# Optimization experiments

Measured on AMD Instinct MI355X. Metric: run time of the kernel, lower is better.

## Reference

```python
import jax, jax.numpy as jnp
import numpy as np

N = 8192
E = 131072
IN_DIM = 3000
HID = 512      # gcn1 out = HID // 2 = 256
OUT = 64
EPS = 1e-12


def gcn_conv(x, W, b, src, dst, n):
    """PyG GCNConv: add self-loops, symmetric norm, gather-matmul-scatter."""
    xw = x @ W                                   # [n, out]
    loop = jnp.arange(n, dtype=src.dtype)
    s = jnp.concatenate([src, loop])             # source j
    d = jnp.concatenate([dst, loop])             # target i
    deg = jax.ops.segment_sum(jnp.ones(s.shape[0], dtype=xw.dtype), d, num_segments=n)
    dinv = deg ** -0.5                           # deg >= 1 due to self-loops
    norm = dinv[s] * dinv[d]                     # [E+n]
    out = jax.ops.segment_sum(norm[:, None] * xw[s], d, num_segments=n)
    return out + b


def avg_readout(emb, mask):
    vsum = mask @ emb                            # [N, h]
    row_sum = jnp.sum(mask, axis=1, keepdims=True)
    g = vsum / row_sum
    nrm = jnp.maximum(jnp.linalg.norm(g, axis=1, keepdims=True), EPS)
    return g / nrm                               # F.normalize(p=2, dim=1)


def bilinear(h, c, Wd, bd):
    # nn.Bilinear(n_h, n_h, 1): out[n,o] = sum_ij h[n,i] Wd[o,i,j] c[n,j] + bd[o]
    return jnp.einsum('ni,oij,nj->no', h, Wd, c) + bd


def setup_inputs() -> dict:
    key = jax.random.key(0)
    k1, k2, k3, k4, k5, k6, k7 = jax.random.split(key, 7)
    gene_data = jax.random.normal(k1, (N, IN_DIM), dtype=jnp.float32)
    # sparse binary neighborhood mask (~16 neighbors/row) + self so row sums > 0
    mask = (jax.random.uniform(k2, (N, N)) < (16.0 / N)).astype(jnp.float32)
    mask = jnp.maximum(mask, jnp.eye(N, dtype=jnp.float32))
    spatial_edge_index = jax.random.randint(k3, (2, E), 0, N, dtype=jnp.int64)
    perm = jax.random.permutation(k4, N).astype(jnp.int64)
    h1 = HID // 2
    W1 = jax.random.normal(k5, (IN_DIM, h1), dtype=jnp.float32) / np.sqrt(IN_DIM)
    b1 = jnp.zeros((h1,), dtype=jnp.float32)
    W2 = jax.random.normal(k6, (h1, OUT), dtype=jnp.float32) / np.sqrt(h1)
    b2 = jnp.zeros((OUT,), dtype=jnp.float32)
    Wd = jax.random.normal(k7, (1, OUT, OUT), dtype=jnp.float32) / np.sqrt(OUT)
    bd = jnp.zeros((1,), dtype=jnp.float32)
    return {"gene_data": gene_data, "mask": mask, "W1": W1, "b1": b1,
            "W2": W2, "b2": b2, "Wd": Wd, "bd": bd,
            "spatial_edge_index": spatial_edge_index, "perm": perm}


def reference(gene_data, mask, W1, b1, W2, b2, Wd, bd, spatial_edge_index, perm):
    src, dst = spatial_edge_index[0], spatial_edge_index[1]
    n = gene_data.shape[0]
    x1 = gene_data
    x1_c = gene_data[perm]                       # permuted (corrupted) graph
    # dropout inactive (eval mode, p=0.0)
    x1 = jax.nn.relu(gcn_conv(x1, W1, b1, src, dst, n))
    x1_c = jax.nn.relu(gcn_conv(x1_c, W1, b1, src, dst, n))
    x1 = jax.nn.relu(gcn_conv(x1, W2, b2, src, dst, n))
    x1_c = jax.nn.relu(gcn_conv(x1_c, W2, b2, src, dst, n))
    g1 = jax.nn.sigmoid(avg_readout(x1, mask))
    g1_c = jax.nn.sigmoid(avg_readout(x1_c, mask))
    ret1 = jnp.concatenate([bilinear(x1, g1, Wd, bd), bilinear(x1_c, g1, Wd, bd)], axis=1)
    ret1_c = jnp.concatenate([bilinear(x1_c, g1_c, Wd, bd), bilinear(x1, g1_c, Wd, bd)], axis=1)
    return (x1, ret1, ret1_c)
```

## Files before the change

kernel.cpp:

```cpp
#include <hip/hip_runtime.h>
#include <hip/hip_bf16.h>

#define NN 8192
#define NMASK 8191
#define IND 3000
#define H1 256
#define OUTD 64

typedef __bf16 bf16x8 __attribute__((ext_vector_type(8)));
typedef float floatx4 __attribute__((ext_vector_type(4)));

__device__ __forceinline__ unsigned short f2b(float f) {
    __hip_bfloat16 h = __float2bfloat16(f);
    unsigned short u;
    __builtin_memcpy(&u, &h, 2);
    return u;
}


__global__ void k_probe(float code, float* out) {
    if (threadIdx.x == 0 && blockIdx.x == 0) out[0] = code;
}


__global__ void k_detect64(const unsigned* __restrict__ raw, int pairs, int* __restrict__ flag) {
    __shared__ int cnt;
    if (threadIdx.x == 0) cnt = 0;
    __syncthreads();
    int z = 0;
    for (int k = threadIdx.x; k < pairs; k += blockDim.x)
        if (raw[2 * k + 1] == 0u) z++;
    atomicAdd(&cnt, z);
    __syncthreads();
    if (threadIdx.x == 0) *flag = (cnt > pairs / 2) ? 1 : 0;
}

__global__ void k_norm_idx(const unsigned* __restrict__ raw, const int* __restrict__ flag,
                           int* __restrict__ out, int count) {
    int i = blockIdx.x * blockDim.x + threadIdx.x;
    if (i < count) {
        unsigned v = (*flag) ? raw[2 * (size_t)i] : raw[i];
        out[i] = (int)(v & (unsigned)NMASK);
    }
}


__global__ void k_degree(const int* __restrict__ dst, int* __restrict__ deg, int E) {
    int e = blockIdx.x * blockDim.x + threadIdx.x;
    if (e < E) atomicAdd(&deg[dst[e]], 1);
}

__global__ __launch_bounds__(1024) void k_scan(const int* __restrict__ deg,
                                               int* __restrict__ row_ptr,
                                               int* __restrict__ cursor,
                                               float* __restrict__ dinv, int n) {
    __shared__ int sums[1024];
    int t = threadIdx.x;
    int per = n / 1024;
    int base = t * per;
    int s = 0;
    for (int u = 0; u < per; ++u) s += deg[base + u];
    sums[t] = s;
    __syncthreads();
    for (int off = 1; off < 1024; off <<= 1) {
        int v = (t >= off) ? sums[t - off] : 0;
        __syncthreads();
        sums[t] += v;
        __syncthreads();
    }
    int run = (t == 0) ? 0 : sums[t - 1];
    for (int u = 0; u < per; ++u) {
        int i = base + u;
        row_ptr[i] = run;
        cursor[i] = run;
        int d = deg[i];
        dinv[i] = rsqrtf((float)(1 + d));
        run += d;
    }
    if (t == 1023) row_ptr[n] = run;
}

__global__ void k_scatter(const int* __restrict__ src, const int* __restrict__ dst,
                          int* __restrict__ cursor, int* __restrict__ col, int E) {
    int e = blockIdx.x * blockDim.x + threadIdx.x;
    if (e < E) {
        int d = dst[e];
        int p = atomicAdd(&cursor[d], 1);
        if (p >= 0 && p < E) col[p] = src[e];
    }
}

__global__ void k_transpose_f2b(const float* __restrict__ in,
                                __hip_bfloat16* __restrict__ out, int R, int C) {
    int idx = blockIdx.x * blockDim.x + threadIdx.x;
    if (idx < R * C) {
        int r = idx / C, c = idx % C;
        out[(size_t)c * R + r] = __float2bfloat16(in[idx]);
    }
}


template <int AFP32>
__global__ __launch_bounds__(256) void k_gemm_bt(const void* __restrict__ Araw,
                                                 const __hip_bfloat16* __restrict__ Bt,
                                                 float* __restrict__ C,
                                                 int M, int N, int K) {
    __shared__ __align__(16) unsigned short As[64 * 40];
    __shared__ __align__(16) unsigned short Bs[64 * 40];
    int t = threadIdx.x;
    int m0 = blockIdx.x * 64;
    int n0 = blockIdx.y * 64;
    int lane = t & 63;
    int w = t >> 6;
    int srow = t >> 2;
    int schunk = (t & 3) * 8;
    size_t aoff = (size_t)(m0 + srow) * K + schunk;
    const unsigned short* Brow = (const unsigned short*)Bt + (size_t)(n0 + srow) * K + schunk;

    floatx4 acc0 = {0.f, 0.f, 0.f, 0.f}, acc1 = acc0, acc2 = acc0, acc3 = acc0;
    int msub = w * 16;
    int arow = msub + (lane & 15);
    int koff = (lane >> 4) * 8;
    int nlo = lane & 15;

    for (int k0 = 0; k0 < K; k0 += 32) {
        uint4 av = make_uint4(0u, 0u, 0u, 0u);
        uint4 bv = make_uint4(0u, 0u, 0u, 0u);
        if (k0 + schunk < K) {
            if (AFP32) {
                const float* ap = (const float*)Araw + aoff + k0;
                float4 f0 = *reinterpret_cast<const float4*>(ap);
                float4 f1 = *reinterpret_cast<const float4*>(ap + 4);
                unsigned short t8[8] = {f2b(f0.x), f2b(f0.y), f2b(f0.z), f2b(f0.w),
                                        f2b(f1.x), f2b(f1.y), f2b(f1.z), f2b(f1.w)};
                __builtin_memcpy(&av, t8, 16);
            } else {
                av = *reinterpret_cast<const uint4*>((const unsigned short*)Araw + aoff + k0);
            }
            bv = *reinterpret_cast<const uint4*>(Brow + k0);
        }
        __syncthreads();
        *reinterpret_cast<uint4*>(&As[srow * 40 + schunk]) = av;
        *reinterpret_cast<uint4*>(&Bs[srow * 40 + schunk]) = bv;
        __syncthreads();
        bf16x8 af = *reinterpret_cast<const bf16x8*>(&As[arow * 40 + koff]);
        bf16x8 bf0 = *reinterpret_cast<const bf16x8*>(&Bs[(0 + nlo) * 40 + koff]);
        bf16x8 bf1 = *reinterpret_cast<const bf16x8*>(&Bs[(16 + nlo) * 40 + koff]);
        bf16x8 bf2 = *reinterpret_cast<const bf16x8*>(&Bs[(32 + nlo) * 40 + koff]);
        bf16x8 bf3 = *reinterpret_cast<const bf16x8*>(&Bs[(48 + nlo) * 40 + koff]);
        acc0 = __builtin_amdgcn_mfma_f32_16x16x32_bf16(af, bf0, acc0, 0, 0, 0);
        acc1 = __builtin_amdgcn_mfma_f32_16x16x32_bf16(af, bf1, acc1, 0, 0, 0);
        acc2 = __builtin_amdgcn_mfma_f32_16x16x32_bf16(af, bf2, acc2, 0, 0, 0);
        acc3 = __builtin_amdgcn_mfma_f32_16x16x32_bf16(af, bf3, acc3, 0, 0, 0);
    }
    int crow = msub + (lane >> 4) * 4;
    int ccol = lane & 15;
    floatx4 accs[4] = {acc0, acc1, acc2, acc3};
#pragma unroll
    for (int j = 0; j < 4; ++j) {
#pragma unroll
        for (int r = 0; r < 4; ++r) {
            C[(size_t)(m0 + crow + r) * N + (n0 + j * 16 + ccol)] = accs[j][r];
        }
    }
}


__global__ __launch_bounds__(256) void k_agg1(const float* __restrict__ xw1,
                                              const int* __restrict__ row_ptr,
                                              const int* __restrict__ col,
                                              const float* __restrict__ dinv,
                                              const int* __restrict__ perm,
                                              const float* __restrict__ b1,
                                              __hip_bfloat16* __restrict__ h_all, int n) {
    __shared__ int colS[64];
    __shared__ int pcolS[64];
    __shared__ float wS[64];
    int i = blockIdx.x;
    int c = threadIdx.x;
    float di = dinv[i];
    int pi = perm[i];
    float sw = di * di;
    float acc = sw * xw1[(size_t)i * H1 + c];
    float accc = sw * xw1[(size_t)pi * H1 + c];
    int s = row_ptr[i], e = row_ptr[i + 1];
    for (int base = s; base < e; base += 64) {
        int cnt = min(64, e - base);
        __syncthreads();
        if (c < cnt) {
            int j = col[base + c];
            colS[c] = j;
            wS[c] = di * dinv[j];
            pcolS[c] = perm[j];
        }
        __syncthreads();
#pragma unroll 4
        for (int u = 0; u < cnt; ++u) {
            float wv = wS[u];
            acc += wv * xw1[(size_t)colS[u] * H1 + c];
            accc += wv * xw1[(size_t)pcolS[u] * H1 + c];
        }
    }
    float b = b1[c];
    h_all[(size_t)i * H1 + c] = __float2bfloat16(fmaxf(acc + b, 0.f));
    h_all[(size_t)(n + i) * H1 + c] = __float2bfloat16(fmaxf(accc + b, 0.f));
}


__global__ __launch_bounds__(256) void k_agg2(const float* __restrict__ hw_all,
                                              const int* __restrict__ row_ptr,
                                              const int* __restrict__ col,
                                              const float* __restrict__ dinv,
                                              const float* __restrict__ b2,
                                              float* __restrict__ x1_all,
                                              float* __restrict__ out_x1, int n) {
    int lane = threadIdx.x & 63;
    int i = blockIdx.x * 4 + (threadIdx.x >> 6);
    float di = dinv[i];
    float sw = di * di;
    float acc = sw * hw_all[(size_t)i * OUTD + lane];
    float accc = sw * hw_all[(size_t)(n + i) * OUTD + lane];
    int s = row_ptr[i], e = row_ptr[i + 1];
    for (int t = s; t < e; ++t) {
        int j = col[t];
        float wv = di * dinv[j];
        acc += wv * hw_all[(size_t)j * OUTD + lane];
        accc += wv * hw_all[(size_t)(n + j) * OUTD + lane];
    }
    float b = b2[lane];
    float v = fmaxf(acc + b, 0.f);
    float vc = fmaxf(accc + b, 0.f);
    x1_all[(size_t)i * OUTD + lane] = v;
    x1_all[(size_t)(n + i) * OUTD + lane] = vc;
    out_x1[(size_t)i * OUTD + lane] = v;
}


__global__ __launch_bounds__(256) void k_readout(const float* __restrict__ mask,
                                                 const float* __restrict__ x1_all,
                                                 float* __restrict__ g_all, int n) {
    int i = blockIdx.x;
    int lane = threadIdx.x & 63;
    int w = threadIdx.x >> 6;
    float acc = 0.f, accc = 0.f, rs = 0.f;
    const float* mrow = mask + (size_t)i * n;
    int quarter = n >> 2;
    int qbase = w * quarter;
    int iters = quarter / 256;
    for (int it = 0; it < iters; ++it) {
        int jb = qbase + it * 256 + lane * 4;
        float4 q = *reinterpret_cast<const float4*>(mrow + jb);
        bool nz = (q.x != 0.f) || (q.y != 0.f) || (q.z != 0.f) || (q.w != 0.f);
        unsigned long long bal = __ballot(nz);
        while (bal) {
            int l = __builtin_ctzll(bal);
            bal &= bal - 1;
            float s0 = __shfl(q.x, l), s1 = __shfl(q.y, l);
            float s2 = __shfl(q.z, l), s3 = __shfl(q.w, l);
            int j0 = qbase + it * 256 + l * 4;
            float sv[4] = {s0, s1, s2, s3};
#pragma unroll
            for (int u = 0; u < 4; ++u) {
                if (sv[u] != 0.f) {
                    float m = sv[u];
                    int j = j0 + u;
                    acc += m * x1_all[(size_t)j * OUTD + lane];
                    accc += m * x1_all[(size_t)(n + j) * OUTD + lane];
                    rs += m;
                }
            }
        }
    }
    __shared__ float sa[4][64], sc[4][64], sr[4];
    sa[w][lane] = acc;
    sc[w][lane] = accc;
    if (lane == 0) sr[w] = rs;
    __syncthreads();
    if (w == 0) {
        float tot = sa[0][lane] + sa[1][lane] + sa[2][lane] + sa[3][lane];
        float totc = sc[0][lane] + sc[1][lane] + sc[2][lane] + sc[3][lane];
        float rst = fmaxf(sr[0] + sr[1] + sr[2] + sr[3], 1e-20f);
        float g = tot / rst;
        float gc = totc / rst;
        float s1 = g * g, s2 = gc * gc;
#pragma unroll
        for (int off = 32; off; off >>= 1) {
            s1 += __shfl_xor(s1, off);
            s2 += __shfl_xor(s2, off);
        }
        float gn = g / fmaxf(sqrtf(s1), 1e-12f);
        float gnc = gc / fmaxf(sqrtf(s2), 1e-12f);
        g_all[(size_t)i * OUTD + lane] = 1.f / (1.f + __expf(-gn));
        g_all[(size_t)(n + i) * OUTD + lane] = 1.f / (1.f + __expf(-gnc));
    }
}


__global__ __launch_bounds__(256) void k_bilinear(const float* __restrict__ x1_all,
                                                  const float* __restrict__ g_all,
                                                  const float* __restrict__ Wd,
                                                  const float* __restrict__ bd,
                                                  float* __restrict__ out_ret1,
                                                  float* __restrict__ out_ret1c, int n) {
    __shared__ float WdS[64][65];
    __shared__ float gS[4][64], gcS[4][64];
    int t = threadIdx.x;
    for (int u = t; u < 64 * 64; u += 256) WdS[u >> 6][u & 63] = Wd[u];
    int lane = t & 63;
    int q = t >> 6;
    int i = blockIdx.x * 4 + q;
    float g = g_all[(size_t)i * OUTD + lane];
    float gc = g_all[(size_t)(n + i) * OUTD + lane];
    gS[q][lane] = g;
    gcS[q][lane] = gc;
    __syncthreads();
    float tg = 0.f, tgc = 0.f;
#pragma unroll 8
    for (int j = 0; j < 64; ++j) {
        float wv = WdS[lane][j];
        tg += wv * gS[q][j];
        tgc += wv * gcS[q][j];
    }
    float x = x1_all[(size_t)i * OUTD + lane];
    float xc = x1_all[(size_t)(n + i) * OUTD + lane];
    float r0 = x * tg, r1 = xc * tg, r2 = xc * tgc, r3 = x * tgc;
#pragma unroll
    for (int off = 32; off; off >>= 1) {
        r0 += __shfl_down(r0, off);
        r1 += __shfl_down(r1, off);
        r2 += __shfl_down(r2, off);
        r3 += __shfl_down(r3, off);
    }
    if (lane == 0) {
        float b = bd[0];
        out_ret1[(size_t)i * 2 + 0] = r0 + b;
        out_ret1[(size_t)i * 2 + 1] = r1 + b;
        out_ret1c[(size_t)i * 2 + 0] = r2 + b;
        out_ret1c[(size_t)i * 2 + 1] = r3 + b;
    }
}


extern "C" void kernel_launch(void* const* d_in, const int* in_sizes, int n_in,
                              void* d_out, int out_size, void* d_ws, size_t ws_size,
                              hipStream_t stream) {
    const float* gene = (const float*)d_in[0];
    const float* mask = (const float*)d_in[1];
    const float* W1 = (const float*)d_in[2];
    const float* b1 = (const float*)d_in[3];
    const float* W2 = (const float*)d_in[4];
    const float* b2 = (const float*)d_in[5];
    const float* Wd = (const float*)d_in[6];
    const float* bd = (const float*)d_in[7];
    const unsigned* eidx_raw = (const unsigned*)d_in[8];
    const unsigned* perm_raw = (const unsigned*)d_in[9];
    const int n = NN;
    const int E = in_sizes[8] / 2;

    char* base = (char*)d_ws;
    char* p = base;
    auto alloc = [&](size_t bytes) -> char* {
        char* r = p;
        p += (bytes + 255) & ~(size_t)255;
        return r;
    };
    int* flags = (int*)alloc(256);
    int* eidx32 = (int*)alloc((size_t)2 * E * 4);
    int* perm32 = (int*)alloc((size_t)n * 4);
    int* deg = (int*)alloc((size_t)n * 4);
    int* row_ptr = (int*)alloc((size_t)(n + 1) * 4);
    int* cursor = (int*)alloc((size_t)n * 4);
    float* dinv = (float*)alloc((size_t)n * 4);
    int* col = (int*)alloc((size_t)E * 4);
    __hip_bfloat16* W2t = (__hip_bfloat16*)alloc((size_t)H1 * OUTD * 2);
    __hip_bfloat16* W1t = (__hip_bfloat16*)alloc((size_t)IND * H1 * 2);
    float* xw1 = (float*)alloc((size_t)n * H1 * 4);
    __hip_bfloat16* h_all = (__hip_bfloat16*)alloc((size_t)2 * n * H1 * 2);
    size_t need = (size_t)(p - base);
    float* hw_all = xw1;
    float* x1_all = xw1 + (size_t)2 * n * OUTD;
    float* g_all = (float*)h_all;

    float* out_x1 = (float*)d_out;
    float* out_ret1 = out_x1 + (size_t)n * OUTD;
    float* out_ret1c = out_ret1 + (size_t)n * 2;

    if (ws_size < need) {
        k_probe<<<1, 64, 0, stream>>>(1000.f + (float)(ws_size >> 20), out_x1);
        return;
    }

    hipMemsetAsync(flags, 0, 256, stream);
    hipMemsetAsync(deg, 0, (size_t)n * 4, stream);

    k_detect64<<<1, 256, 0, stream>>>(eidx_raw, 2048, &flags[0]);
    k_detect64<<<1, 256, 0, stream>>>(perm_raw, 2048, &flags[1]);
    k_norm_idx<<<(2 * E + 255) / 256, 256, 0, stream>>>(eidx_raw, &flags[0], eidx32, 2 * E);
    k_norm_idx<<<(n + 255) / 256, 256, 0, stream>>>(perm_raw, &flags[1], perm32, n);
    const int* srcv = eidx32;
    const int* dstv = eidx32 + E;

    k_degree<<<(E + 255) / 256, 256, 0, stream>>>(dstv, deg, E);
    k_scan<<<1, 1024, 0, stream>>>(deg, row_ptr, cursor, dinv, n);
    k_scatter<<<(E + 255) / 256, 256, 0, stream>>>(srcv, dstv, cursor, col, E);

    k_transpose_f2b<<<(IND * H1 + 255) / 256, 256, 0, stream>>>(W1, W1t, IND, H1);
    k_transpose_f2b<<<(H1 * OUTD + 255) / 256, 256, 0, stream>>>(W2, W2t, H1, OUTD);

    k_gemm_bt<1><<<dim3(n / 64, H1 / 64), 256, 0, stream>>>(gene, W1t, xw1, n, H1, IND);

    k_agg1<<<n, H1, 0, stream>>>(xw1, row_ptr, col, dinv, perm32, b1, h_all, n);

    k_gemm_bt<0><<<dim3(2 * n / 64, OUTD / 64), 256, 0, stream>>>(h_all, W2t, hw_all, 2 * n, OUTD, H1);

    k_agg2<<<n / 4, 256, 0, stream>>>(hw_all, row_ptr, col, dinv, b2, x1_all, out_x1, n);

    k_readout<<<n, 256, 0, stream>>>(mask, x1_all, g_all, n);

    k_bilinear<<<n / 4, 256, 0, stream>>>(x1_all, g_all, Wd, bd, out_ret1, out_ret1c, n);
}
```

Before: 634.5 us.

## Widen GEMM K-tile, tile weight transpose, prefetch readout mask, fuse index setup kernels

The bf16 MFMA GEMM now stages 64-wide K tiles instead of 32, which halves the number of barrier round-trips and doubles the MFMAs issued per shared-memory fill. The weight transpose now goes through a padded 64x64 shared-memory tile so both reads and writes are coalesced. The readout kernel issues all eight float4 mask loads up front before processing any of them, to hide memory latency. Index preprocessing is also trimmed: the two detect kernels become one launch, degree counting is folded into edge normalisation, and the two memsets are merged into one, which cuts launch count at the cost of more register and LDS use.

```diff
diff --git a/kernel.cpp b/kernel.cpp
--- a/kernel.cpp
+++ b/kernel.cpp
@@ -23,20 +23,33 @@
 }
 
 
-__global__ void k_detect64(const unsigned* __restrict__ raw, int pairs, int* __restrict__ flag) {
+__global__ void k_detect_both(const unsigned* __restrict__ e, const unsigned* __restrict__ p,
+                              int* __restrict__ flags) {
+    const unsigned* raw = blockIdx.x ? p : e;
     __shared__ int cnt;
     if (threadIdx.x == 0) cnt = 0;
     __syncthreads();
     int z = 0;
-    for (int k = threadIdx.x; k < pairs; k += blockDim.x)
+    for (int k = threadIdx.x; k < 2048; k += blockDim.x)
         if (raw[2 * k + 1] == 0u) z++;
     atomicAdd(&cnt, z);
     __syncthreads();
-    if (threadIdx.x == 0) *flag = (cnt > pairs / 2) ? 1 : 0;
-}
-
-__global__ void k_norm_idx(const unsigned* __restrict__ raw, const int* __restrict__ flag,
-                           int* __restrict__ out, int count) {
+    if (threadIdx.x == 0) flags[blockIdx.x] = (cnt > 1024) ? 1 : 0;
+}
+
+__global__ void k_norm_eidx(const unsigned* __restrict__ raw, const int* __restrict__ flag,
+                            int* __restrict__ out, int E, int* __restrict__ deg) {
+    int i = blockIdx.x * blockDim.x + threadIdx.x;
+    if (i < 2 * E) {
+        unsigned v = (*flag) ? raw[2 * (size_t)i] : raw[i];
+        int x = (int)(v & (unsigned)NMASK);
+        out[i] = x;
+        if (i >= E) atomicAdd(&deg[x], 1);
+    }
+}
+
+__global__ void k_norm_perm(const unsigned* __restrict__ raw, const int* __restrict__ flag,
+                            int* __restrict__ out, int count) {
     int i = blockIdx.x * blockDim.x + threadIdx.x;
     if (i < count) {
         unsigned v = (*flag) ? raw[2 * (size_t)i] : raw[i];
@@ -44,11 +57,6 @@
     }
 }
 
-
-__global__ void k_degree(const int* __restrict__ dst, int* __restrict__ deg, int E) {
-    int e = blockIdx.x * blockDim.x + threadIdx.x;
-    if (e < E) atomicAdd(&deg[dst[e]], 1);
-}
 
 __global__ __launch_bounds__(1024) void k_scan(const int* __restrict__ deg,
                                                int* __restrict__ row_ptr,
@@ -90,12 +98,28 @@
     }
 }
 
-__global__ void k_transpose_f2b(const float* __restrict__ in,
-                                __hip_bfloat16* __restrict__ out, int R, int C) {
-    int idx = blockIdx.x * blockDim.x + threadIdx.x;
-    if (idx < R * C) {
-        int r = idx / C, c = idx % C;
-        out[(size_t)c * R + r] = __float2bfloat16(in[idx]);
+
+__global__ __launch_bounds__(256) void k_transpose_f2b_t(const float* __restrict__ in,
+                                                         __hip_bfloat16* __restrict__ out,
+                                                         int R, int C) {
+    __shared__ float tile[64][65];
+    int c0 = blockIdx.x * 64;
+    int r0 = blockIdx.y * 64;
+    int t = threadIdx.x;
+    int tc = t & 63;
+    int tq = t >> 6;
+#pragma unroll
+    for (int s = 0; s < 16; ++s) {
+        int rr = tq + s * 4;
+        int r = r0 + rr;
+        tile[rr][tc] = (r < R) ? in[(size_t)r * C + c0 + tc] : 0.f;
+    }
+    __syncthreads();
+#pragma unroll
+    for (int s = 0; s < 16; ++s) {
+        int cc = tq + s * 4;
+        int r = r0 + tc;
+        if (r < R) out[(size_t)(c0 + cc) * R + r] = __float2bfloat16(tile[tc][cc]);
     }
 }
 
@@ -105,17 +129,15 @@
                                                  const __hip_bfloat16* __restrict__ Bt,
                                                  float* __restrict__ C,
                                                  int M, int N, int K) {
-    __shared__ __align__(16) unsigned short As[64 * 40];
-    __shared__ __align__(16) unsigned short Bs[64 * 40];
+    __shared__ __align__(16) unsigned short As[64 * 72];
+    __shared__ __align__(16) unsigned short Bs[64 * 72];
     int t = threadIdx.x;
     int m0 = blockIdx.x * 64;
     int n0 = blockIdx.y * 64;
     int lane = t & 63;
     int w = t >> 6;
     int srow = t >> 2;
-    int schunk = (t & 3) * 8;
-    size_t aoff = (size_t)(m0 + srow) * K + schunk;
-    const unsigned short* Brow = (const unsigned short*)Bt + (size_t)(n0 + srow) * K + schunk;
+    int kc = (t & 3) * 16;
 
     floatx4 acc0 = {0.f, 0.f, 0.f, 0.f}, acc1 = acc0, acc2 = acc0, acc3 = acc0;
     int msub = w * 16;
@@ -123,35 +145,47 @@
     int koff = (lane >> 4) * 8;
     int nlo = lane & 15;
 
-    for (int k0 = 0; k0 < K; k0 += 32) {
-        uint4 av = make_uint4(0u, 0u, 0u, 0u);
-        uint4 bv = make_uint4(0u, 0u, 0u, 0u);
-        if (k0 + schunk < K) {
-            if (AFP32) {
-                const float* ap = (const float*)Araw + aoff + k0;
-                float4 f0 = *reinterpret_cast<const float4*>(ap);
-                float4 f1 = *reinterpret_cast<const float4*>(ap + 4);
-                unsigned short t8[8] = {f2b(f0.x), f2b(f0.y), f2b(f0.z), f2b(f0.w),
-                                        f2b(f1.x), f2b(f1.y), f2b(f1.z), f2b(f1.w)};
-                __builtin_memcpy(&av, t8, 16);
-            } else {
-                av = *reinterpret_cast<const uint4*>((const unsigned short*)Araw + aoff + k0);
+    for (int k0 = 0; k0 < K; k0 += 64) {
+        unsigned short a16[16] = {0};
+        unsigned short b16[16] = {0};
+#pragma unroll
+        for (int h = 0; h < 2; ++h) {
+            int kk = k0 + kc + h * 8;
+            if (kk < K) {
+                if (AFP32) {
+                    const float* ap = (const float*)Araw + (size_t)(m0 + srow) * K + kk;
+                    float4 f0 = *reinterpret_cast<const float4*>(ap);
+                    float4 f1 = *reinterpret_cast<const float4*>(ap + 4);
+                    a16[h * 8 + 0] = f2b(f0.x); a16[h * 8 + 1] = f2b(f0.y);
+                    a16[h * 8 + 2] = f2b(f0.z); a16[h * 8 + 3] = f2b(f0.w);
+                    a16[h * 8 + 4] = f2b(f1.x); a16[h * 8 + 5] = f2b(f1.y);
+                    a16[h * 8 + 6] = f2b(f1.z); a16[h * 8 + 7] = f2b(f1.w);
+                } else {
+                    uint4 v = *reinterpret_cast<const uint4*>(
+                        (const unsigned short*)Araw + (size_t)(m0 + srow) * K + kk);
+                    __builtin_memcpy(&a16[h * 8], &v, 16);
+                }
+                uint4 bvv = *reinterpret_cast<const uint4*>(
+                    (const unsigned short*)Bt + (size_t)(n0 + srow) * K + kk);
+                __builtin_memcpy(&b16[h * 8], &bvv, 16);
             }
-            bv = *reinterpret_cast<const uint4*>(Brow + k0);
-        }
-        __syncthreads();
-        *reinterpret_cast<uint4*>(&As[srow * 40 + schunk]) = av;
-        *reinterpret_cast<uint4*>(&Bs[srow * 40 + schunk]) = bv;
-        __syncthreads();
-        bf16x8 af = *reinterpret_cast<const bf16x8*>(&As[arow * 40 + koff]);
-        bf16x8 bf0 = *reinterpret_cast<const bf16x8*>(&Bs[(0 + nlo) * 40 + koff]);
-        bf16x8 bf1 = *reinterpret_cast<const bf16x8*>(&Bs[(16 + nlo) * 40 + koff]);
-        bf16x8 bf2 = *reinterpret_cast<const bf16x8*>(&Bs[(32 + nlo) * 40 + koff]);
-        bf16x8 bf3 = *reinterpret_cast<const bf16x8*>(&Bs[(48 + nlo) * 40 + koff]);
-        acc0 = __builtin_amdgcn_mfma_f32_16x16x32_bf16(af, bf0, acc0, 0, 0, 0);
-        acc1 = __builtin_amdgcn_mfma_f32_16x16x32_bf16(af, bf1, acc1, 0, 0, 0);
-        acc2 = __builtin_amdgcn_mfma_f32_16x16x32_bf16(af, bf2, acc2, 0, 0, 0);
-        acc3 = __builtin_amdgcn_mfma_f32_16x16x32_bf16(af, bf3, acc3, 0, 0, 0);
+        }
+        __syncthreads();
+        *reinterpret_cast<uint4*>(&As[srow * 72 + kc]) = *reinterpret_cast<uint4*>(&a16[0]);
+        *reinterpret_cast<uint4*>(&As[srow * 72 + kc + 8]) = *reinterpret_cast<uint4*>(&a16[8]);
+        *reinterpret_cast<uint4*>(&Bs[srow * 72 + kc]) = *reinterpret_cast<uint4*>(&b16[0]);
+        *reinterpret_cast<uint4*>(&Bs[srow * 72 + kc + 8]) = *reinterpret_cast<uint4*>(&b16[8]);
+        __syncthreads();
+        bf16x8 a0 = *reinterpret_cast<const bf16x8*>(&As[arow * 72 + koff]);
+        bf16x8 a1 = *reinterpret_cast<const bf16x8*>(&As[arow * 72 + 32 + koff]);
+#pragma unroll
+        for (int j = 0; j < 4; ++j) {
+            bf16x8 b0 = *reinterpret_cast<const bf16x8*>(&Bs[(j * 16 + nlo) * 72 + koff]);
+            bf16x8 b1 = *reinterpret_cast<const bf16x8*>(&Bs[(j * 16 + nlo) * 72 + 32 + koff]);
+            floatx4* ac = (j == 0) ? &acc0 : (j == 1) ? &acc1 : (j == 2) ? &acc2 : &acc3;
+            *ac = __builtin_amdgcn_mfma_f32_16x16x32_bf16(a0, b0, *ac, 0, 0, 0);
+            *ac = __builtin_amdgcn_mfma_f32_16x16x32_bf16(a1, b1, *ac, 0, 0, 0);
+        }
     }
     int crow = msub + (lane >> 4) * 4;
     int ccol = lane & 15;
@@ -244,19 +278,20 @@
     int w = threadIdx.x >> 6;
     float acc = 0.f, accc = 0.f, rs = 0.f;
     const float* mrow = mask + (size_t)i * n;
-    int quarter = n >> 2;
-    int qbase = w * quarter;
-    int iters = quarter / 256;
-    for (int it = 0; it < iters; ++it) {
-        int jb = qbase + it * 256 + lane * 4;
-        float4 q = *reinterpret_cast<const float4*>(mrow + jb);
-        bool nz = (q.x != 0.f) || (q.y != 0.f) || (q.z != 0.f) || (q.w != 0.f);
+    int qbase = w * (n >> 2);
+    float4 q[8];
+#pragma unroll
+    for (int it = 0; it < 8; ++it)
+        q[it] = *reinterpret_cast<const float4*>(mrow + qbase + it * 256 + lane * 4);
+#pragma unroll
+    for (int it = 0; it < 8; ++it) {
+        bool nz = (q[it].x != 0.f) || (q[it].y != 0.f) || (q[it].z != 0.f) || (q[it].w != 0.f);
         unsigned long long bal = __ballot(nz);
         while (bal) {
             int l = __builtin_ctzll(bal);
             bal &= bal - 1;
-            float s0 = __shfl(q.x, l), s1 = __shfl(q.y, l);
-            float s2 = __shfl(q.z, l), s3 = __shfl(q.w, l);
+            float s0 = __shfl(q[it].x, l), s1 = __shfl(q[it].y, l);
+            float s2 = __shfl(q[it].z, l), s3 = __shfl(q[it].w, l);
             int j0 = qbase + it * 256 + l * 4;
             float sv[4] = {s0, s1, s2, s3};
 #pragma unroll
@@ -365,9 +400,9 @@
         return r;
     };
     int* flags = (int*)alloc(256);
+    int* deg = (int*)alloc((size_t)n * 4);
     int* eidx32 = (int*)alloc((size_t)2 * E * 4);
     int* perm32 = (int*)alloc((size_t)n * 4);
-    int* deg = (int*)alloc((size_t)n * 4);
     int* row_ptr = (int*)alloc((size_t)(n + 1) * 4);
     int* cursor = (int*)alloc((size_t)n * 4);
     float* dinv = (float*)alloc((size_t)n * 4);
@@ -390,22 +425,19 @@
         return;
     }
 
-    hipMemsetAsync(flags, 0, 256, stream);
-    hipMemsetAsync(deg, 0, (size_t)n * 4, stream);
-
-    k_detect64<<<1, 256, 0, stream>>>(eidx_raw, 2048, &flags[0]);
-    k_detect64<<<1, 256, 0, stream>>>(perm_raw, 2048, &flags[1]);
-    k_norm_idx<<<(2 * E + 255) / 256, 256, 0, stream>>>(eidx_raw, &flags[0], eidx32, 2 * E);
-    k_norm_idx<<<(n + 255) / 256, 256, 0, stream>>>(perm_raw, &flags[1], perm32, n);
+    hipMemsetAsync(flags, 0, 256 + (size_t)n * 4, stream);
+
+    k_detect_both<<<2, 256, 0, stream>>>(eidx_raw, perm_raw, flags);
+    k_norm_eidx<<<(2 * E + 255) / 256, 256, 0, stream>>>(eidx_raw, &flags[0], eidx32, E, deg);
+    k_norm_perm<<<(n + 255) / 256, 256, 0, stream>>>(perm_raw, &flags[1], perm32, n);
     const int* srcv = eidx32;
     const int* dstv = eidx32 + E;
 
-    k_degree<<<(E + 255) / 256, 256, 0, stream>>>(dstv, deg, E);
     k_scan<<<1, 1024, 0, stream>>>(deg, row_ptr, cursor, dinv, n);
     k_scatter<<<(E + 255) / 256, 256, 0, stream>>>(srcv, dstv, cursor, col, E);
 
-    k_transpose_f2b<<<(IND * H1 + 255) / 256, 256, 0, stream>>>(W1, W1t, IND, H1);
-    k_transpose_f2b<<<(H1 * OUTD + 255) / 256, 256, 0, stream>>>(W2, W2t, H1, OUTD);
+    k_transpose_f2b_t<<<dim3(H1 / 64, (IND + 63) / 64), 256, 0, stream>>>(W1, W1t, IND, H1);
+    k_transpose_f2b_t<<<dim3(OUTD / 64, (H1 + 63) / 64), 256, 0, stream>>>(W2, W2t, H1, OUTD);
 
     k_gemm_bt<1><<<dim3(n / 64, H1 / 64), 256, 0, stream>>>(gene, W1t, xw1, n, H1, IND);
 
```

Measured after the change: 636.4 us. No clear change (+0.3%).
